# Kernel optimization log

Hardware: AMD Instinct MI355X
Metric: run time of the kernel (lower is better)

The kernel has to match this reference:

```python
import jax, jax.numpy as jnp
import numpy as np

RADIUS = 0.3
NSAMPLE = 16
NPOINT = 256
EPS = 1e-5


def setup_inputs() -> dict:
    key = jax.random.key(0)
    ks = jax.random.split(key, 12)
    B, N, C = 16, 16384, 288
    d = {
        "xyz": jax.random.uniform(ks[0], (B, N, 3), jnp.float32),
        "features": jax.random.normal(ks[1], (B, C, N), jnp.float32),
    }
    cin = [C + 3, C, C]  # use_xyz adds 3 to first SharedMLP width
    for i in range(3):
        d[f"W{i}"] = jax.random.normal(ks[2 + i], (C, cin[i]), jnp.float32) / np.float32(np.sqrt(cin[i]))
        d[f"g{i}"] = jnp.ones((C,), jnp.float32)
        d[f"b{i}"] = jnp.zeros((C,), jnp.float32)
        d[f"m{i}"] = jax.random.normal(ks[5 + i], (C,), jnp.float32) * 0.1
        d[f"v{i}"] = jax.random.uniform(ks[8 + i], (C,), jnp.float32, minval=0.5, maxval=1.5)
    return d


def fps(xyz, npoint):
    """Farthest point sampling. xyz: (B,N,3) -> inds (B,npoint) int32."""
    B, N, _ = xyz.shape
    d0 = jnp.full((B, N), 1e10, xyz.dtype)
    i0 = jnp.zeros((B,), jnp.int32)  # CUDA kernel starts from index 0

    def step(carry, _):
        dist, idx = carry
        cur = jnp.take_along_axis(xyz, idx[:, None, None], axis=1)  # (B,1,3)
        d = jnp.sum((xyz - cur) ** 2, axis=-1)  # (B,N)
        dist = jnp.minimum(dist, d)
        nxt = jnp.argmax(dist, axis=-1).astype(jnp.int32)
        return (dist, nxt), idx

    _, inds = jax.lax.scan(step, (d0, i0), None, length=npoint)
    return inds.T  # (B, npoint)


def ball_query(xyz, new_xyz):
    """xyz: (B,N,3), new_xyz: (B,S,3) -> idx (B,S,NSAMPLE) int32.
    First NSAMPLE in-radius indices; pad with the first found index (CUDA semantics)."""
    N = xyz.shape[1]
    d2 = jnp.sum((new_xyz[:, :, None, :] - xyz[:, None, :, :]) ** 2, axis=-1)  # (B,S,N)
    mask = d2 < RADIUS * RADIUS
    cand = jnp.where(mask, jnp.arange(N, dtype=jnp.int32), jnp.int32(N))
    cand = jnp.sort(cand, axis=-1)[..., :NSAMPLE]
    first = cand[..., :1]
    return jnp.where(cand == N, first, cand)


def _mlp_bn_relu(h, W, g, b, m, v):
    # 1x1 Conv2d (no bias) + BatchNorm (running stats) + ReLU on (B,C,S,K)
    h = jnp.einsum('oc,bcsk->bosk', W, h)
    scale = (g * jax.lax.rsqrt(v + EPS))[:, None, None]
    return jax.nn.relu((h - m[:, None, None]) * scale + b[:, None, None])


def reference(xyz, features, W0, g0, b0, m0, v0, W1, g1, b1, m1, v1, W2, g2, b2, m2, v2):
    inds = fps(xyz, NPOINT)                                   # (B,S)
    new_xyz = jax.vmap(lambda p, i: p[i])(xyz, inds)          # (B,S,3)
    idx = ball_query(xyz, new_xyz)                            # (B,S,K)
    g_xyz = jax.vmap(lambda p, i: p[i])(xyz, idx)             # (B,S,K,3)
    g_xyz = (g_xyz - new_xyz[:, :, None, :]) / RADIUS         # normalize_xyz
    g_feat = jax.vmap(lambda f, i: f[:, i])(features, idx)    # (B,C,S,K)
    h = jnp.concatenate([jnp.transpose(g_xyz, (0, 3, 1, 2)), g_feat], axis=1)  # (B,C+3,S,K)
    for (W, g, b, m, v) in ((W0, g0, b0, m0, v0), (W1, g1, b1, m1, v1), (W2, g2, b2, m2, v2)):
        h = _mlp_bn_relu(h, W, g, b, m, v)
    new_features = jnp.max(h, axis=-1)                        # (B,C,S) max-pool over nsample
    return new_xyz, new_features, inds
```

## Files before the change

kernel.cpp:

```cpp
#include <hip/hip_runtime.h>
#include <hip/hip_bf16.h>
#include <string.h>

#define NPT   16384
#define NBAT  16
#define CH    288
#define SP    256
#define KS    16
#define OFF_FEAT 12288L
#define OFF_IND  1191936L

__device__ __forceinline__ float bfbits(unsigned short u){
  unsigned int x = ((unsigned int)u) << 16; float f; __builtin_memcpy(&f,&x,4); return f;
}
__device__ __forceinline__ float ldf(const void* p, long i, int isb){
  if (isb) return __bfloat162float(((const __hip_bfloat16*)p)[i]);
  return ((const float*)p)[i];
}
__device__ __forceinline__ void sto(void* p, long i, float v, int isb){
  if (isb) ((__hip_bfloat16*)p)[i] = __float2bfloat16(v);
  else     ((float*)p)[i] = v;
}
__device__ __forceinline__ void gload_lds(const void* g, void* l){
  __builtin_amdgcn_global_load_lds((const __attribute__((address_space(1))) void*)g,
      (__attribute__((address_space(3))) void*)l, 16, 0, 0);
}
__device__ __forceinline__ unsigned spread4(unsigned x){
  return (x&1u) | ((x&2u)<<2) | ((x&4u)<<4) | ((x&8u)<<6);
}

typedef __attribute__((ext_vector_type(8))) short bf16x8;
typedef __attribute__((ext_vector_type(4))) float f32x4;
typedef __attribute__((ext_vector_type(2))) float f32x2;

template<int CTRL>
__device__ __forceinline__ unsigned long long ror_max64(unsigned long long k){
  int lo2 = __builtin_amdgcn_update_dpp(0, (int)(unsigned)k, CTRL, 0xf, 0xf, false);
  int hi2 = __builtin_amdgcn_update_dpp(0, (int)(unsigned)(k>>32), CTRL, 0xf, 0xf, false);
  unsigned long long o = ((unsigned long long)(unsigned)hi2 << 32) | (unsigned)lo2;
  return o > k ? o : k;
}
__device__ __forceinline__ unsigned long long rowmax64(unsigned long long k){
  k = ror_max64<0x121>(k);
  k = ror_max64<0x122>(k);
  k = ror_max64<0x124>(k);
  k = ror_max64<0x128>(k);
  return k;
}
__device__ __forceinline__ unsigned long long rl64(unsigned long long v, int l){
  unsigned lo = (unsigned)__builtin_amdgcn_readlane((int)(unsigned)v, l);
  unsigned hi = (unsigned)__builtin_amdgcn_readlane((int)(unsigned)(v>>32), l);
  return (((unsigned long long)hi)<<32) | lo;
}

__global__ void detect_k(const void* __restrict__ xyz, int* __restrict__ flag){
  __shared__ float red[256];
  const int t = threadIdx.x;
  const unsigned short* u = (const unsigned short*)xyz;
  float m = 0.f;
  for (int i = t; i < 4096; i += 256){
    float f = fabsf(bfbits(u[i]));
    if (f != f) f = 1e30f;
    m = fmaxf(m, f);
  }
  red[t] = m; __syncthreads();
  for (int s = 128; s; s >>= 1){ if (t < s) red[t] = fmaxf(red[t], red[t+s]); __syncthreads(); }
  if (t == 0) *flag = (red[0] < 2.0f) ? 1 : 0;
}

__global__ __launch_bounds__(256) void cvtxyz_k(const void* __restrict__ xyz,
    const int* __restrict__ flag, float* __restrict__ X, float* __restrict__ Y,
    float* __restrict__ Z, float4* __restrict__ P4){
  const int n = blockIdx.x*256 + threadIdx.x;
  const int isb = *flag;
  float x = ldf(xyz, (long)n*3+0, isb);
  float y = ldf(xyz, (long)n*3+1, isb);
  float z = ldf(xyz, (long)n*3+2, isb);
  X[n] = x; Y[n] = y; Z[n] = z;
  P4[n] = make_float4(x, y, z, 0.f);
}

__global__ __launch_bounds__(256) void cvtw_k(const void* __restrict__ W,
    const void* __restrict__ g, const void* __restrict__ bb,
    const void* __restrict__ m, const void* __restrict__ v,
    const int* __restrict__ flag, __hip_bfloat16* __restrict__ Wbf,
    float* __restrict__ scale, float* __restrict__ shift, int Kin){
  const int isb = *flag;
  const int idx = blockIdx.x*256 + threadIdx.x;
  if (idx < 288*296){
    int o = idx / 296, k = idx - o*296;
    float val = (k < Kin) ? ldf(W, (long)o*Kin + k, isb) : 0.f;
    Wbf[idx] = __float2bfloat16(val);
  }
  if (idx < 288){
    float sc = ldf(g, idx, isb) * rsqrtf(ldf(v, idx, isb) + 1e-5f);
    scale[idx] = sc;
    shift[idx] = ldf(bb, idx, isb) - ldf(m, idx, isb)*sc;
  }
}

__global__ __launch_bounds__(1024) void sort_k(const float* __restrict__ X,
    const float* __restrict__ Y, const float* __restrict__ Z,
    float* __restrict__ X2, float* __restrict__ Y2, float* __restrict__ Z2,
    int* __restrict__ I2){
  __shared__ int hist[4096];
  __shared__ int wtot[16];
  const int b = blockIdx.x, t = threadIdx.x, base = b*NPT;
  for (int j = t; j < 4096; j += 1024) hist[j] = 0;
  __syncthreads();
  int cell[16]; float lx[16], ly[16], lz[16];
  #pragma unroll
  for (int i=0;i<16;i++){
    const int id = t + i*1024;
    float x = X[base+id], y = Y[base+id], z = Z[base+id];
    lx[i]=x; ly[i]=y; lz[i]=z;
    int cx = (int)(x*16.f); cx = cx<0?0:(cx>15?15:cx);
    int cy = (int)(y*16.f); cy = cy<0?0:(cy>15?15:cy);
    int cz = (int)(z*16.f); cz = cz<0?0:(cz>15?15:cz);
    cell[i] = (int)(spread4((unsigned)cx) | (spread4((unsigned)cy)<<1) | (spread4((unsigned)cz)<<2));
    atomicAdd(&hist[cell[i]], 1);
  }
  __syncthreads();
  int s0 = hist[t*4], s1 = hist[t*4+1], s2 = hist[t*4+2], s3 = hist[t*4+3];
  int ls = s0+s1+s2+s3;
  int sc = ls;
  #pragma unroll
  for (int off=1; off<64; off<<=1){
    int o = __shfl_up(sc, off, 64);
    if ((t&63) >= off) sc += o;
  }
  if ((t&63) == 63) wtot[t>>6] = sc;
  __syncthreads();
  int wpre = 0;
  #pragma unroll
  for (int w=0; w<16; w++) wpre += (w < (t>>6)) ? wtot[w] : 0;
  const int ebase = wpre + sc - ls;
  hist[t*4]   = ebase;
  hist[t*4+1] = ebase + s0;
  hist[t*4+2] = ebase + s0 + s1;
  hist[t*4+3] = ebase + s0 + s1 + s2;
  __syncthreads();
  #pragma unroll
  for (int i=0;i<16;i++){
    const int dst = atomicAdd(&hist[cell[i]], 1);
    X2[base+dst] = lx[i]; Y2[base+dst] = ly[i]; Z2[base+dst] = lz[i];
    I2[base+dst] = t + i*1024;
  }
}

__global__ __launch_bounds__(1024) __attribute__((amdgpu_waves_per_eu(4,4)))
void fps_k(const float4* __restrict__ P4,
    const float* __restrict__ X2, const float* __restrict__ Y2,
    const float* __restrict__ Z2, const int* __restrict__ I2,
    const int* __restrict__ flag, float* __restrict__ nxyz, void* __restrict__ dout){
  #pragma clang fp contract(off)
  const int b = blockIdx.x, t = threadIdx.x;
  const int base = b*NPT;
  const int lane = t & 63, wid = t >> 6;
  f32x2 px[8], py[8], pz[8], ds[8];
  unsigned li2[8];
  unsigned long long pk[8];
  const int p0 = base + wid*1024 + lane;
  #pragma unroll
  for (int j=0;j<8;j++){
    px[j] = (f32x2){X2[p0 + (2*j)*64], X2[p0 + (2*j+1)*64]};
    py[j] = (f32x2){Y2[p0 + (2*j)*64], Y2[p0 + (2*j+1)*64]};
    pz[j] = (f32x2){Z2[p0 + (2*j)*64], Z2[p0 + (2*j+1)*64]};
    unsigned a = 16383u - (unsigned)I2[p0 + (2*j)*64];
    unsigned c = 16383u - (unsigned)I2[p0 + (2*j+1)*64];
    li2[j] = a | (c<<16);
    ds[j] = (f32x2){1e10f, 1e10f};
    pk[j] = 0ull;
  }
  float pnx=0.f, pxx=0.f, pny=0.f, pxy=0.f, pnz=0.f, pxz=0.f;
  const int myp = lane & 7;
  #pragma unroll
  for (int j=0;j<8;j++){
    float nx = fminf(px[j].x,px[j].y), xx = fmaxf(px[j].x,px[j].y);
    float ny = fminf(py[j].x,py[j].y), xy = fmaxf(py[j].x,py[j].y);
    float nz = fminf(pz[j].x,pz[j].y), xz = fmaxf(pz[j].x,pz[j].y);
    #pragma unroll
    for (int off=32; off; off>>=1){
      nx = fminf(nx, __shfl_xor(nx, off, 64)); xx = fmaxf(xx, __shfl_xor(xx, off, 64));
      ny = fminf(ny, __shfl_xor(ny, off, 64)); xy = fmaxf(xy, __shfl_xor(xy, off, 64));
      nz = fminf(nz, __shfl_xor(nz, off, 64)); xz = fmaxf(xz, __shfl_xor(xz, off, 64));
    }
    if (myp == j){ pnx=nx; pxx=xx; pny=ny; pxy=xy; pnz=nz; pxz=xz; }
  }
  __shared__ unsigned long long slot[2][16];
  __shared__ float ox[SP], oy[SP], oz[SP];
  __shared__ int   oi[SP];
  float4 c4 = P4[base];
  float cx = c4.x, cy = c4.y, cz = c4.z;
  int cur = 0;
  unsigned long long wk = 0ull;
  float wavemax = 1e30f;
  for (int it=0; it<SP; it++){
    if (t == 0){ ox[it]=cx; oy[it]=cy; oz[it]=cz; oi[it]=cur; }
    float ddx = fmaxf(fmaxf(pnx-cx, cx-pxx), 0.f);
    float ddy = fmaxf(fmaxf(pny-cy, cy-pxy), 0.f);
    float ddz = fmaxf(fmaxf(pnz-cz, cz-pxz), 0.f);
    float lb = ddx*ddx + ddy*ddy; lb = lb + ddz*ddz;
    unsigned mask = (unsigned)__ballot(!(lb * 0.9999f > wavemax)) & 0xffu;
    mask = (unsigned)__builtin_amdgcn_readfirstlane((int)mask);
    if (mask){
      const f32x2 Cx = {cx,cx}, Cy = {cy,cy}, Cz = {cz,cz};
      #define UPD(j) if (mask & (1u<<(j))) { \
        f32x2 dx = px[j]-Cx, dy = py[j]-Cy, dz = pz[j]-Cz; \
        f32x2 m0 = dx*dx, m1 = dy*dy, m2 = dz*dz; \
        f32x2 d2 = (m0+m1)+m2; \
        f32x2 dn = __builtin_elementwise_min(ds[j], d2); \
        ds[j] = dn; \
        unsigned long long k0 = ((unsigned long long)__float_as_uint(dn.x)<<32) | (unsigned long long)(li2[j] & 0xFFFFu); \
        unsigned long long k1 = ((unsigned long long)__float_as_uint(dn.y)<<32) | (unsigned long long)(li2[j] >> 16); \
        pk[j] = (k0 > k1) ? k0 : k1; }
      UPD(0) UPD(1) UPD(2) UPD(3) UPD(4) UPD(5) UPD(6) UPD(7)
      #undef UPD
      unsigned long long best = pk[0];
      #pragma unroll
      for (int j=1;j<8;j++) best = (pk[j] > best) ? pk[j] : best;
      best = rowmax64(best);
      unsigned long long r0 = rl64(best, 0),  r1 = rl64(best, 16);
      unsigned long long r2 = rl64(best, 32), r3 = rl64(best, 48);
      unsigned long long a01 = (r0 > r1) ? r0 : r1;
      unsigned long long a23 = (r2 > r3) ? r2 : r3;
      wk = (a01 > a23) ? a01 : a23;
      wavemax = __uint_as_float((unsigned)(wk >> 32));
    }
    const int p = it & 1;
    if (lane == 0) slot[p][wid] = wk;
    __syncthreads();
    unsigned long long g = slot[p][lane & 15];
    g = rowmax64(g);
    cur = 16383 - (int)(unsigned)g;
    cur = __builtin_amdgcn_readfirstlane(cur);
    c4 = P4[base+cur];
    cx = c4.x; cy = c4.y; cz = c4.z;
  }
  __syncthreads();
  if (t < SP){
    const int isb = *flag;
    const long bs = (long)b*SP + t;
    float fx=ox[t], fy=oy[t], fz=oz[t]; int ii=oi[t];
    nxyz[bs*3+0]=fx; nxyz[bs*3+1]=fy; nxyz[bs*3+2]=fz;
    sto(dout, bs*3+0, fx, isb);
    sto(dout, bs*3+1, fy, isb);
    sto(dout, bs*3+2, fz, isb);
    sto(dout, OFF_IND + bs, (float)ii, isb);
  }
}

__global__ __launch_bounds__(256) void ballq_k(const float* __restrict__ X,
    const float* __restrict__ Y, const float* __restrict__ Z,
    const float* __restrict__ nxyz, int* __restrict__ bidx){
  #pragma clang fp contract(off)
  const int gw = (blockIdx.x*256 + threadIdx.x) >> 6;
  const int lane = threadIdx.x & 63;
  const int b = gw >> 8, base = b*NPT;
  const float cx = nxyz[gw*3+0], cy = nxyz[gw*3+1], cz = nxyz[gw*3+2];
  int cnt = 0, first = 0; bool havef = false;
  for (int st = 0; st < NPT && cnt < KS; st += 64){
    const int id = st + lane;
    float dx = X[base+id]-cx, dy = Y[base+id]-cy, dz = Z[base+id]-cz;
    float d2 = dx*dx + dy*dy; d2 = d2 + dz*dz;
    unsigned long long mk = __ballot(d2 <= 0.09f);
    if (mk){
      if (!havef){ first = st + __builtin_ctzll(mk); havef = true; }
      int rank = cnt + __popcll(mk & ((1ull<<lane)-1ull));
      if (((mk>>lane)&1ull) && rank < KS) bidx[gw*KS + rank] = id;
      cnt += __popcll(mk);
    }
  }
  if (cnt < KS && lane >= cnt && lane < KS) bidx[gw*KS + lane] = first;
}

__global__ __launch_bounds__(256) void gather_k(const void* __restrict__ xyz,
    const void* __restrict__ feat, const int* __restrict__ flag,
    const int* __restrict__ bidx, const float* __restrict__ nxyz,
    __hip_bfloat16* __restrict__ h0){
  __shared__ __hip_bfloat16 tile[64*296];
  const int isb = *flag;
  const int t = threadIdx.x, n0 = blockIdx.x*64;
  const int nl = t >> 2, cg = t & 3;
  const int n = n0 + nl, b = n >> 12, s = n >> 4;
  const int id = bidx[n];
  for (int j=0; j<74; j++){
    int c = cg*74 + j;
    float vv = 0.f;
    if (c < 3)       vv = (ldf(xyz, ((long)b*NPT + id)*3 + c, isb) - nxyz[(long)s*3 + c]) / 0.3f;
    else if (c < 291) vv = ldf(feat, ((long)b*CH + (c-3))*(long)NPT + id, isb);
    tile[nl*296 + c] = __float2bfloat16(vv);
  }
  __syncthreads();
  const uint4* src = (const uint4*)tile;
  uint4* dst = (uint4*)((char*)h0 + (long)n0*592);
  for (int j = t; j < 2368; j += 256) dst[j] = src[j];
}

__global__ __launch_bounds__(256, 2) void gemm_k(
    const __hip_bfloat16* __restrict__ A, int astr,
    const __hip_bfloat16* __restrict__ W,
    const float* __restrict__ scale, const float* __restrict__ shift,
    __hip_bfloat16* __restrict__ Out, int ostr,
    int ktiles, int kvalid){
  extern __shared__ char lds[];
  const int t = threadIdx.x, lane = t & 63, wid = t >> 6;
  const int wm = wid & 1, wo = wid >> 1;
  const int bx = blockIdx.x, by = blockIdx.y;
  {
    const char* src = (const char*)(A + (long)bx*128*astr);
    const int chunks = (128*astr*2) >> 10;
    for (int c = wid; c < chunks; c += 4)
      gload_lds(src + c*1024 + lane*16, lds + c*1024);
  }
  f32x4 acc[4][3];
  #pragma unroll
  for (int mf=0; mf<4; mf++)
    #pragma unroll
    for (int of=0; of<3; of++) acc[mf][of] = (f32x4){0.f,0.f,0.f,0.f};

  const int mrow  = wm*64 + (lane & 15);
  const int kg    = (lane >> 4) * 8;
  const int obase = by*96 + wo*48 + (lane & 15);
  __syncthreads();

  for (int kt = 0; kt < ktiles; kt++){
    const int k0 = kt*32 + kg;
    const bool z = (k0 >= kvalid);
    const int k0c = z ? 0 : k0;
    bf16x8 a[4], bf[3];
    #pragma unroll
    for (int mf=0; mf<4; mf++)
      a[mf] = *(const bf16x8*)(lds + ((long)(mrow + mf*16)*astr + k0c)*2);
    if (z){
      bf16x8 zz = {0,0,0,0,0,0,0,0};
      #pragma unroll
      for (int mf=0; mf<4; mf++) a[mf] = zz;
    }
    #pragma unroll
    for (int of=0; of<3; of++)
      bf[of] = *(const bf16x8*)(W + (long)(obase + of*16)*296 + k0c);
    #pragma unroll
    for (int mf=0; mf<4; mf++)
      #pragma unroll
      for (int of=0; of<3; of++)
        acc[mf][of] = __builtin_amdgcn_mfma_f32_16x16x32_bf16(a[mf], bf[of], acc[mf][of], 0, 0, 0);
  }

  float sc[3], sh[3];
  #pragma unroll
  for (int of=0; of<3; of++){ sc[of] = scale[obase + of*16]; sh[of] = shift[obase + of*16]; }
  #pragma unroll
  for (int mf=0; mf<4; mf++)
    #pragma unroll
    for (int of=0; of<3; of++)
      #pragma unroll
      for (int r=0; r<4; r++){
        const long row = (long)bx*128 + wm*64 + mf*16 + (lane>>4)*4 + r;
        const int o = obase + of*16;
        float vv = acc[mf][of][r]*sc[of] + sh[of];
        Out[row*ostr + o] = __float2bfloat16(fmaxf(vv, 0.f));
      }
}

__global__ __launch_bounds__(256) void maxk_k(const __hip_bfloat16* __restrict__ h,
    const int* __restrict__ flag, void* __restrict__ dout){
  __shared__ __hip_bfloat16 tile[128*288];
  const int isb = *flag;
  const int t = threadIdx.x;
  const int b = blockIdx.x >> 5, s0 = (blockIdx.x & 31)*8;
  const long n0 = (long)b*4096 + (long)s0*16;
  {
    const char* src = (const char*)(h + n0*288);
    for (int c = (t>>6); c < 72; c += 4)
      gload_lds(src + c*1024 + (t&63)*16, (char*)tile + c*1024);
  }
  __syncthreads();
  for (int o = t; o < 288; o += 256){
    float mx[8];
    #pragma unroll
    for (int sl=0; sl<8; sl++){
      float m = -1e30f;
      #pragma unroll
      for (int kk=0; kk<16; kk++)
        m = fmaxf(m, __bfloat162float(tile[(sl*16 + kk)*288 + o]));
      mx[sl] = m;
    }
    const long e0 = OFF_FEAT + (long)b*73728 + (long)o*256 + s0;
    if (isb){
      unsigned short u[8];
      #pragma unroll
      for (int sl=0; sl<8; sl++){
        __hip_bfloat16 hb = __float2bfloat16(mx[sl]);
        __builtin_memcpy(&u[sl], &hb, 2);
      }
      uint4 pk; __builtin_memcpy(&pk, u, 16);
      *(uint4*)((__hip_bfloat16*)dout + e0) = pk;
    } else {
      float* fo = (float*)dout + e0;
      *(float4*)fo     = make_float4(mx[0],mx[1],mx[2],mx[3]);
      *(float4*)(fo+4) = make_float4(mx[4],mx[5],mx[6],mx[7]);
    }
  }
}

extern "C" void kernel_launch(void* const* d_in, const int* in_sizes, int n_in,
                              void* d_out, int out_size, void* d_ws, size_t ws_size,
                              hipStream_t stream){
  const void* xyz  = d_in[0];
  const void* feat = d_in[1];
  const void* W0 = d_in[2];  const void* g0 = d_in[3];  const void* b0 = d_in[4];
  const void* m0 = d_in[5];  const void* v0 = d_in[6];
  const void* W1 = d_in[7];  const void* g1 = d_in[8];  const void* b1 = d_in[9];
  const void* m1 = d_in[10]; const void* v1 = d_in[11];
  const void* W2 = d_in[12]; const void* g2 = d_in[13]; const void* b2 = d_in[14];
  const void* m2 = d_in[15]; const void* v2 = d_in[16];

  char* ws = (char*)d_ws;
  int*   flag  = (int*)ws;
  float* sc0   = (float*)(ws + 64);
  float* sh0   = sc0 + 288;
  float* sc1   = sc0 + 576;  float* sh1 = sc0 + 864;
  float* sc2   = sc0 + 1152; float* sh2 = sc0 + 1440;
  __hip_bfloat16* Wb0 = (__hip_bfloat16*)(ws + 7040);
  __hip_bfloat16* Wb1 = Wb0 + 288*296;
  __hip_bfloat16* Wb2 = Wb1 + 288*296;
  float* nxyz = (float*)(ws + 518656);
  int*   bidx = (int*)(ws + 567808);
  float* X    = (float*)(ws + 1048576);
  float* Y    = X + NBAT*NPT;
  float* Z    = Y + NBAT*NPT;
  float4* P4  = (float4*)(ws + 1048576 + 3145728);
  __hip_bfloat16* bufA = (__hip_bfloat16*)(ws + 1048576);
  __hip_bfloat16* bufB = (__hip_bfloat16*)(ws + 1048576 + 38797312);
  float* X2 = (float*)bufB;
  float* Y2 = X2 + NBAT*NPT;
  float* Z2 = Y2 + NBAT*NPT;
  int*   I2 = (int*)(Z2 + NBAT*NPT);

  detect_k<<<1, 256, 0, stream>>>(xyz, flag);
  cvtxyz_k<<<1024, 256, 0, stream>>>(xyz, flag, X, Y, Z, P4);
  cvtw_k<<<333, 256, 0, stream>>>(W0, g0, b0, m0, v0, flag, Wb0, sc0, sh0, 291);
  cvtw_k<<<333, 256, 0, stream>>>(W1, g1, b1, m1, v1, flag, Wb1, sc1, sh1, 288);
  cvtw_k<<<333, 256, 0, stream>>>(W2, g2, b2, m2, v2, flag, Wb2, sc2, sh2, 288);
  sort_k<<<NBAT, 1024, 0, stream>>>(X, Y, Z, X2, Y2, Z2, I2);
  fps_k<<<NBAT, 1024, 0, stream>>>(P4, X2, Y2, Z2, I2, flag, nxyz, d_out);
  ballq_k<<<1024, 256, 0, stream>>>(X, Y, Z, nxyz, bidx);
  gather_k<<<1024, 256, 0, stream>>>(xyz, feat, flag, bidx, nxyz, bufA);
  gemm_k<<<dim3(512,3), 256, 128*296*2, stream>>>(bufA, 296, Wb0, sc0, sh0, bufB, 288, 10, 296);
  gemm_k<<<dim3(512,3), 256, 128*288*2, stream>>>(bufB, 288, Wb1, sc1, sh1, bufA, 296, 9, 288);
  gemm_k<<<dim3(512,3), 256, 128*296*2, stream>>>(bufA, 296, Wb2, sc2, sh2, bufB, 288, 9, 288);
  maxk_k<<<512, 256, 0, stream>>>(bufB, flag, d_out);
}
```

Before: 934.9 us.

## Gather features via inverted index with coalesced tile loads; pass FPS winner coords through LDS

The feature gather now builds an inverted index of ball-query hits grouped into 64-point buckets. Each block reads a contiguous 288x64 feature tile with coalesced loads and scatters rows to every sample that references those points, replacing the per-sample strided column reads. FPS no longer fetches the chosen point from global memory after each reduction. The winning wave publishes its point's coordinates in shared memory instead, which removes a dependent global load from the serial loop. This adds an extra index-building kernel, and every block now reads its whole tile even when few samples reference it.

```diff
diff --git a/kernel.cpp b/kernel.cpp
--- a/kernel.cpp
+++ b/kernel.cpp
@@ -70,14 +70,13 @@
 
 __global__ __launch_bounds__(256) void cvtxyz_k(const void* __restrict__ xyz,
     const int* __restrict__ flag, float* __restrict__ X, float* __restrict__ Y,
-    float* __restrict__ Z, float4* __restrict__ P4){
+    float* __restrict__ Z){
   const int n = blockIdx.x*256 + threadIdx.x;
   const int isb = *flag;
   float x = ldf(xyz, (long)n*3+0, isb);
   float y = ldf(xyz, (long)n*3+1, isb);
   float z = ldf(xyz, (long)n*3+2, isb);
   X[n] = x; Y[n] = y; Z[n] = z;
-  P4[n] = make_float4(x, y, z, 0.f);
 }
 
 __global__ __launch_bounds__(256) void cvtw_k(const void* __restrict__ W,
@@ -149,7 +148,8 @@
 }
 
 __global__ __launch_bounds__(1024) __attribute__((amdgpu_waves_per_eu(4,4)))
-void fps_k(const float4* __restrict__ P4,
+void fps_k(const float* __restrict__ X, const float* __restrict__ Y,
+    const float* __restrict__ Z,
     const float* __restrict__ X2, const float* __restrict__ Y2,
     const float* __restrict__ Z2, const int* __restrict__ I2,
     const int* __restrict__ flag, float* __restrict__ nxyz, void* __restrict__ dout){
@@ -188,12 +188,13 @@
     if (myp == j){ pnx=nx; pxx=xx; pny=ny; pxy=xy; pnz=nz; pxz=xz; }
   }
   __shared__ unsigned long long slot[2][16];
+  __shared__ float4 slotc[2][16];
   __shared__ float ox[SP], oy[SP], oz[SP];
   __shared__ int   oi[SP];
-  float4 c4 = P4[base];
-  float cx = c4.x, cy = c4.y, cz = c4.z;
+  float cx = X[base], cy = Y[base], cz = Z[base];
   int cur = 0;
-  unsigned long long wk = 0ull;
+  unsigned long long wk = 0ull, best = 0ull;
+  int bj = 0;
   float wavemax = 1e30f;
   for (int it=0; it<SP; it++){
     if (t == 0){ ox[it]=cx; oy[it]=cy; oz[it]=cz; oi[it]=cur; }
@@ -216,12 +217,12 @@
         pk[j] = (k0 > k1) ? k0 : k1; }
       UPD(0) UPD(1) UPD(2) UPD(3) UPD(4) UPD(5) UPD(6) UPD(7)
       #undef UPD
-      unsigned long long best = pk[0];
-      #pragma unroll
-      for (int j=1;j<8;j++) best = (pk[j] > best) ? pk[j] : best;
-      best = rowmax64(best);
-      unsigned long long r0 = rl64(best, 0),  r1 = rl64(best, 16);
-      unsigned long long r2 = rl64(best, 32), r3 = rl64(best, 48);
+      best = pk[0]; bj = 0;
+      #pragma unroll
+      for (int j=1;j<8;j++){ if (pk[j] > best){ best = pk[j]; bj = j; } }
+      unsigned long long rbest = rowmax64(best);
+      unsigned long long r0 = rl64(rbest, 0),  r1 = rl64(rbest, 16);
+      unsigned long long r2 = rl64(rbest, 32), r3 = rl64(rbest, 48);
       unsigned long long a01 = (r0 > r1) ? r0 : r1;
       unsigned long long a23 = (r2 > r3) ? r2 : r3;
       wk = (a01 > a23) ? a01 : a23;
@@ -229,13 +230,24 @@
     }
     const int p = it & 1;
     if (lane == 0) slot[p][wid] = wk;
+    if (best == wk){
+      unsigned long long k0 = ((unsigned long long)__float_as_uint(ds[bj].x)<<32)
+                            | (unsigned long long)(li2[bj] & 0xFFFFu);
+      bool ex = (k0 == wk);
+      slotc[p][wid] = make_float4(ex ? px[bj].x : px[bj].y,
+                                  ex ? py[bj].x : py[bj].y,
+                                  ex ? pz[bj].x : pz[bj].y, 0.f);
+    }
     __syncthreads();
-    unsigned long long g = slot[p][lane & 15];
-    g = rowmax64(g);
+    unsigned long long sv = slot[p][lane & 15];
+    unsigned long long g = rowmax64(sv);
+    unsigned long long wb = __ballot(sv == g);
+    int w = ((int)__builtin_ctzll(wb)) & 15;
+    w = __builtin_amdgcn_readfirstlane(w);
+    float4 cc = slotc[p][w];
     cur = 16383 - (int)(unsigned)g;
     cur = __builtin_amdgcn_readfirstlane(cur);
-    c4 = P4[base+cur];
-    cx = c4.x; cy = c4.y; cz = c4.z;
+    cx = cc.x; cy = cc.y; cz = cc.z;
   }
   __syncthreads();
   if (t < SP){
@@ -274,27 +286,91 @@
   if (cnt < KS && lane >= cnt && lane < KS) bidx[gw*KS + lane] = first;
 }
 
-__global__ __launch_bounds__(256) void gather_k(const void* __restrict__ xyz,
-    const void* __restrict__ feat, const int* __restrict__ flag,
-    const int* __restrict__ bidx, const float* __restrict__ nxyz,
-    __hip_bfloat16* __restrict__ h0){
-  __shared__ __hip_bfloat16 tile[64*296];
+__global__ __launch_bounds__(1024) void invb_k(const int* __restrict__ bidx,
+    int* __restrict__ inv, int* __restrict__ bstart){
+  __shared__ int hist[256];
+  __shared__ int off[256];
+  const int b = blockIdx.x, t = threadIdx.x;
+  if (t < 256) hist[t] = 0;
+  __syncthreads();
+  int id_[4];
+  #pragma unroll
+  for (int i=0;i<4;i++){
+    id_[i] = bidx[b*4096 + t + i*1024];
+    atomicAdd(&hist[id_[i] >> 6], 1);
+  }
+  __syncthreads();
+  if (t < 64){
+    int h0=hist[t*4], h1=hist[t*4+1], h2=hist[t*4+2], h3=hist[t*4+3];
+    int ls = h0+h1+h2+h3, sc = ls;
+    #pragma unroll
+    for (int o=1; o<64; o<<=1){
+      int ov = __shfl_up(sc, o, 64);
+      if (t >= o) sc += ov;
+    }
+    int excl = sc - ls;
+    off[t*4]   = excl;
+    off[t*4+1] = excl + h0;
+    off[t*4+2] = excl + h0 + h1;
+    off[t*4+3] = excl + h0 + h1 + h2;
+    bstart[b*256 + t*4]   = b*4096 + excl;
+    bstart[b*256 + t*4+1] = b*4096 + excl + h0;
+    bstart[b*256 + t*4+2] = b*4096 + excl + h0 + h1;
+    bstart[b*256 + t*4+3] = b*4096 + excl + h0 + h1 + h2;
+  }
+  if (b == 0 && t == 0) bstart[4096] = 65536;
+  __syncthreads();
+  #pragma unroll
+  for (int i=0;i<4;i++){
+    const int sl = t + i*1024;
+    const int pos = atomicAdd(&off[id_[i] >> 6], 1);
+    inv[b*4096 + pos] = sl | (id_[i] << 12);
+  }
+}
+
+__global__ __launch_bounds__(256) void gath2_k(const void* __restrict__ feat,
+    const void* __restrict__ xyz, const int* __restrict__ flag,
+    const int* __restrict__ inv, const int* __restrict__ bstart,
+    const float* __restrict__ nxyz, __hip_bfloat16* __restrict__ h0){
+  __shared__ __hip_bfloat16 tile[CH*66];
   const int isb = *flag;
-  const int t = threadIdx.x, n0 = blockIdx.x*64;
-  const int nl = t >> 2, cg = t & 3;
-  const int n = n0 + nl, b = n >> 12, s = n >> 4;
-  const int id = bidx[n];
-  for (int j=0; j<74; j++){
-    int c = cg*74 + j;
-    float vv = 0.f;
-    if (c < 3)       vv = (ldf(xyz, ((long)b*NPT + id)*3 + c, isb) - nxyz[(long)s*3 + c]) / 0.3f;
-    else if (c < 291) vv = ldf(feat, ((long)b*CH + (c-3))*(long)NPT + id, isb);
-    tile[nl*296 + c] = __float2bfloat16(vv);
-  }
-  __syncthreads();
-  const uint4* src = (const uint4*)tile;
-  uint4* dst = (uint4*)((char*)h0 + (long)n0*592);
-  for (int j = t; j < 2368; j += 256) dst[j] = src[j];
+  const int bid = blockIdx.x;
+  const int b = bid >> 8, r = bid & 255;
+  const int t = threadIdx.x;
+  const int n0 = r*64, ln = t & 63, c0 = t >> 6;
+  const long fb = (long)b*CH*NPT;
+  for (int c = c0; c < CH; c += 4)
+    tile[c*66 + ln] = __float2bfloat16(ldf(feat, fb + (long)c*NPT + n0 + ln, isb));
+  __syncthreads();
+  const int s0 = bstart[bid], s1 = bstart[bid+1];
+  const int q = t & 3;
+  for (int w0 = s0 + (t>>2); w0 < s1; w0 += 64){
+    const int pv = inv[w0];
+    const int sl = pv & 0xFFF;
+    const int id = pv >> 12;
+    const int col = id & 63;
+    const long s = (long)b*4096 + sl;
+    const int ctr = (int)(s >> 4);
+    uint4* dst = (uint4*)(h0 + s*296);
+    const int cbeg = q*9, cend = (q==3) ? 37 : q*9+9;
+    for (int ch = cbeg; ch < cend; ch++){
+      unsigned short u[8];
+      #pragma unroll
+      for (int e=0;e<8;e++){
+        const int hc = ch*8 + e;
+        unsigned short us = 0;
+        if (hc < 3){
+          float vv = (ldf(xyz, ((long)b*NPT + id)*3 + hc, isb) - nxyz[(long)ctr*3 + hc]) / 0.3f;
+          __hip_bfloat16 hb = __float2bfloat16(vv); __builtin_memcpy(&us,&hb,2);
+        } else if (hc < 291){
+          __hip_bfloat16 hb = tile[(hc-3)*66 + col]; __builtin_memcpy(&us,&hb,2);
+        }
+        u[e] = us;
+      }
+      uint4 pkv; __builtin_memcpy(&pkv, u, 16);
+      dst[ch] = pkv;
+    }
+  }
 }
 
 __global__ __launch_bounds__(256, 2) void gemm_k(
@@ -430,23 +506,25 @@
   float* X    = (float*)(ws + 1048576);
   float* Y    = X + NBAT*NPT;
   float* Z    = Y + NBAT*NPT;
-  float4* P4  = (float4*)(ws + 1048576 + 3145728);
   __hip_bfloat16* bufA = (__hip_bfloat16*)(ws + 1048576);
   __hip_bfloat16* bufB = (__hip_bfloat16*)(ws + 1048576 + 38797312);
   float* X2 = (float*)bufB;
   float* Y2 = X2 + NBAT*NPT;
   float* Z2 = Y2 + NBAT*NPT;
   int*   I2 = (int*)(Z2 + NBAT*NPT);
+  int*   inv    = (int*)bufB;
+  int*   bstart = inv + 65536;
 
   detect_k<<<1, 256, 0, stream>>>(xyz, flag);
-  cvtxyz_k<<<1024, 256, 0, stream>>>(xyz, flag, X, Y, Z, P4);
+  cvtxyz_k<<<1024, 256, 0, stream>>>(xyz, flag, X, Y, Z);
   cvtw_k<<<333, 256, 0, stream>>>(W0, g0, b0, m0, v0, flag, Wb0, sc0, sh0, 291);
   cvtw_k<<<333, 256, 0, stream>>>(W1, g1, b1, m1, v1, flag, Wb1, sc1, sh1, 288);
   cvtw_k<<<333, 256, 0, stream>>>(W2, g2, b2, m2, v2, flag, Wb2, sc2, sh2, 288);
   sort_k<<<NBAT, 1024, 0, stream>>>(X, Y, Z, X2, Y2, Z2, I2);
-  fps_k<<<NBAT, 1024, 0, stream>>>(P4, X2, Y2, Z2, I2, flag, nxyz, d_out);
+  fps_k<<<NBAT, 1024, 0, stream>>>(X, Y, Z, X2, Y2, Z2, I2, flag, nxyz, d_out);
   ballq_k<<<1024, 256, 0, stream>>>(X, Y, Z, nxyz, bidx);
-  gather_k<<<1024, 256, 0, stream>>>(xyz, feat, flag, bidx, nxyz, bufA);
+  invb_k<<<NBAT, 1024, 0, stream>>>(bidx, inv, bstart);
+  gath2_k<<<4096, 256, 0, stream>>>(feat, xyz, flag, inv, bstart, nxyz, bufA);
   gemm_k<<<dim3(512,3), 256, 128*296*2, stream>>>(bufA, 296, Wb0, sc0, sh0, bufB, 288, 10, 296);
   gemm_k<<<dim3(512,3), 256, 128*288*2, stream>>>(bufB, 288, Wb1, sc1, sh1, bufA, 296, 9, 288);
   gemm_k<<<dim3(512,3), 256, 128*296*2, stream>>>(bufA, 296, Wb2, sc2, sh2, bufB, 288, 9, 288);
```

Result: slower. 3.440 ms (+268.0%).
